# Optimization experiments

Measured on AMD Instinct MI355X. Metric: run time of the kernel, lower is better.

The kernel has to match this reference:

```python
import jax, jax.numpy as jnp
import numpy as np

GROUP_SIZE = 8
REQUIRED_ZEROS = 4


def _dorefa_quantize(x, bits):
    # tanh-normalize-round
    t = jnp.tanh(x).astype(jnp.float32)
    y = t / jnp.max(jnp.abs(t))
    delta = float(2 ** (bits - 1) - 1)
    _y = jnp.round(y * delta)

    out_c, in_c, h, w = _y.shape
    if in_c < GROUP_SIZE:
        return _y / delta

    g = in_c // GROUP_SIZE
    keep = GROUP_SIZE - REQUIRED_ZEROS  # keep at most 4 non-zeros per group

    # [out_c, g*8, h, w] -> [out_c, g, h, w, 8] (group axis last for top_k)
    yg = _y[:, : g * GROUP_SIZE].reshape(out_c, g, GROUP_SIZE, h, w)
    yg = jnp.transpose(yg, (0, 1, 3, 4, 2))

    # The torch loop zeroes the smallest-|v| non-zeros until >=4 zeros per
    # group. Equivalently: keep only the `keep` largest-|v| entries of each
    # group (zeros have |v|=0, so groups already having >=4 zeros are
    # unchanged). Fully vectorized via batched top-k + one-hot mask.
    absv = jnp.abs(yg)
    _, idx = jax.lax.top_k(absv, keep)                      # [o,g,h,w,keep]
    mask = jax.nn.one_hot(idx, GROUP_SIZE, dtype=yg.dtype).sum(axis=-2)
    yg = yg * mask                                          # [o,g,h,w,8]

    yg = jnp.transpose(yg, (0, 1, 4, 2, 3)).reshape(out_c, g * GROUP_SIZE, h, w)
    out = jnp.concatenate([yg, _y[:, g * GROUP_SIZE :]], axis=1) if g * GROUP_SIZE < in_c else yg
    return out / delta


def setup_inputs() -> dict:
    key = jax.random.key(0)
    x = jax.random.normal(key, (2048, 2048, 3, 3), dtype=jnp.float32)
    return {"x": x, "bits": 8}


def reference(x, bits):
    return _dorefa_quantize(x, bits)
```

## Files before the change

### kernel.cpp

```cpp
#include <hip/hip_runtime.h>
#include <math.h>

#define HW        9
#define GROUP     8
#define KEEP      4
#define DELTA     127.0f
#define INV_DELTA (1.0f / 127.0f)
#define GB_FLOATS 72

__global__ void maxabs_kernel(const float4* __restrict__ x, unsigned* __restrict__ ws, int n4) {
    __shared__ float red[4];
    float m = 0.0f;
    int stride = gridDim.x * blockDim.x;
    #pragma unroll 4
    for (int i = blockIdx.x * blockDim.x + threadIdx.x; i < n4; i += stride) {
        float4 v = x[i];
        m = fmaxf(m, fmaxf(fmaxf(fabsf(v.x), fabsf(v.y)),
                           fmaxf(fabsf(v.z), fabsf(v.w))));
    }
    #pragma unroll
    for (int off = 32; off > 0; off >>= 1)
        m = fmaxf(m, __shfl_down(m, off, 64));
    int wave = threadIdx.x >> 6;
    if ((threadIdx.x & 63) == 0) red[wave] = m;
    __syncthreads();
    if (threadIdx.x == 0) {
        float b = fmaxf(fmaxf(red[0], red[1]), fmaxf(red[2], red[3]));
        atomicMax(ws, __float_as_uint(b));
    }
}

__device__ __attribute__((noinline)) float ref_rz(float xx, float M) {
    float td = (float)tanh((double)xx);
    float y  = td / M;
    return rintf(y * DELTA);
}

__device__ __forceinline__ float fast_tanh(float x) {
    float ax  = fabsf(x);
    float axc = fminf(ax, 10.0f);
    float E   = __expf(2.0f * axc);
    float num = E - 1.0f;
    float den = E + 1.0f;
    float r0  = __builtin_amdgcn_rcpf(den);
    float r   = r0 * fmaf(-den, r0, 2.0f);
    float tl  = copysignf(num * r, x);
    float s = x * x;
    float p = fmaf(s, 0.0035921280f, -0.0088632358f);
    p = fmaf(s, p, 0.021869488f);
    p = fmaf(s, p, -0.053968254f);
    p = fmaf(s, p, 0.13333334f);
    p = fmaf(s, p, -0.33333334f);
    float ts = fmaf(x * s, p, x);
    return (ax <= 0.5f) ? ts : tl;
}

__global__ void quant_kernel(const float4* __restrict__ x,
                             float4* __restrict__ out,
                             const unsigned* __restrict__ ws,
                             int n_gb) {
    __shared__ float sM, sC;
    if (threadIdx.x == 0) {
        float mm = (float)tanh((double)__uint_as_float(*ws));
        sM = mm;
        sC = (float)(127.0 / (double)mm);
    }
    __syncthreads();
    float M = sM, C = sC;

    int gb = blockIdx.x * blockDim.x + threadIdx.x;
    if (gb >= n_gb) return;

    const float4* p = x   + (size_t)gb * (GB_FLOATS / 4);
    float4*       q = out + (size_t)gb * (GB_FLOATS / 4);

    float f[GB_FLOATS];
    #pragma unroll
    for (int k = 0; k < GB_FLOATS / 4; ++k) {
        float4 v = p[k];
        f[4 * k + 0] = v.x; f[4 * k + 1] = v.y;
        f[4 * k + 2] = v.z; f[4 * k + 3] = v.w;
    }

    #pragma unroll
    for (int hw = 0; hw < HW; ++hw) {
        float v8[GROUP], a8[GROUP];
        #pragma unroll
        for (int j = 0; j < GROUP; ++j) {
            float xx = f[j * HW + hw];
            float t  = fast_tanh(xx);
            float z  = t * C;
            float rz = rintf(z);
            float d  = 0.5f - fabsf(z - rz);
            if (d < fmaf(2e-6f, fabsf(z), 5e-7f))
                rz = ref_rz(xx, M);
            v8[j] = rz;
            a8[j] = fabsf(rz);
        }
        int rank[GROUP] = {0, 0, 0, 0, 0, 0, 0, 0};
        #pragma unroll
        for (int i = 0; i < GROUP; ++i) {
            #pragma unroll
            for (int j = i + 1; j < GROUP; ++j) {
                bool ge = (a8[i] >= a8[j]);
                rank[j] += ge ? 1 : 0;
                rank[i] += ge ? 0 : 1;
            }
        }
        #pragma unroll
        for (int j = 0; j < GROUP; ++j) {
            f[j * HW + hw] = (rank[j] < KEEP) ? (v8[j] * INV_DELTA) : 0.0f;
        }
    }

    #pragma unroll
    for (int k = 0; k < GB_FLOATS / 4; ++k) {
        float4 v;
        v.x = f[4 * k + 0]; v.y = f[4 * k + 1];
        v.z = f[4 * k + 2]; v.w = f[4 * k + 3];
        q[k] = v;
    }
}

extern "C" void kernel_launch(void* const* d_in, const int* in_sizes, int n_in,
                              void* d_out, int out_size, void* d_ws, size_t ws_size,
                              hipStream_t stream) {
    const float* x = (const float*)d_in[0];
    float* out = (float*)d_out;
    unsigned* ws = (unsigned*)d_ws;

    int n = in_sizes[0];
    int n4 = n / 4;
    int n_gb = n / GB_FLOATS;

    hipMemsetAsync(ws, 0, sizeof(unsigned), stream);

    maxabs_kernel<<<2048, 256, 0, stream>>>((const float4*)x, ws, n4);

    int blocks = (n_gb + 255) / 256;
    quant_kernel<<<blocks, 256, 0, stream>>>((const float4*)x, (float4*)out, ws, n_gb);
}
```

Before: 308.3 us.

## Stage quant kernel loads and stores through padded LDS for coalesced access

```diff
diff --git a/kernel.cpp b/kernel.cpp
--- a/kernel.cpp
+++ b/kernel.cpp
@@ -6,7 +6,9 @@
 #define KEEP      4
 #define DELTA     127.0f
 #define INV_DELTA (1.0f / 127.0f)
-#define GB_FLOATS 72
+#define ROW_F4    18
+#define ROW_PAD   19
+#define ROWS      256
 
 __global__ void maxabs_kernel(const float4* __restrict__ x, unsigned* __restrict__ ws, int n4) {
     __shared__ float red[4];
@@ -57,29 +59,35 @@
 
 __global__ void quant_kernel(const float4* __restrict__ x,
                              float4* __restrict__ out,
-                             const unsigned* __restrict__ ws,
-                             int n_gb) {
+                             const unsigned* __restrict__ ws) {
+    __shared__ float4 tile[ROWS * ROW_PAD];
     __shared__ float sM, sC;
     if (threadIdx.x == 0) {
         float mm = (float)tanh((double)__uint_as_float(*ws));
         sM = mm;
         sC = (float)(127.0 / (double)mm);
     }
+
+    int t = threadIdx.x;
+    size_t blk_f4 = (size_t)blockIdx.x * (ROWS * ROW_F4);
+
+    #pragma unroll
+    for (int k = 0; k < ROW_F4; ++k) {
+        int L = k * ROWS + t;
+        float4 v = x[blk_f4 + L];
+        int r = L / ROW_F4;
+        int e = L - r * ROW_F4;
+        tile[r * ROW_PAD + e] = v;
+    }
     __syncthreads();
     float M = sM, C = sC;
 
-    int gb = blockIdx.x * blockDim.x + threadIdx.x;
-    if (gb >= n_gb) return;
-
-    const float4* p = x   + (size_t)gb * (GB_FLOATS / 4);
-    float4*       q = out + (size_t)gb * (GB_FLOATS / 4);
-
-    float f[GB_FLOATS];
+    float f[ROWS ? 72 : 0];
     #pragma unroll
-    for (int k = 0; k < GB_FLOATS / 4; ++k) {
-        float4 v = p[k];
-        f[4 * k + 0] = v.x; f[4 * k + 1] = v.y;
-        f[4 * k + 2] = v.z; f[4 * k + 3] = v.w;
+    for (int e = 0; e < ROW_F4; ++e) {
+        float4 v = tile[t * ROW_PAD + e];
+        f[4 * e + 0] = v.x; f[4 * e + 1] = v.y;
+        f[4 * e + 2] = v.z; f[4 * e + 3] = v.w;
     }
 
     #pragma unroll
@@ -88,8 +96,8 @@
         #pragma unroll
         for (int j = 0; j < GROUP; ++j) {
             float xx = f[j * HW + hw];
-            float t  = fast_tanh(xx);
-            float z  = t * C;
+            float t1 = fast_tanh(xx);
+            float z  = t1 * C;
             float rz = rintf(z);
             float d  = 0.5f - fabsf(z - rz);
             if (d < fmaf(2e-6f, fabsf(z), 5e-7f))
@@ -114,11 +122,20 @@
     }
 
     #pragma unroll
-    for (int k = 0; k < GB_FLOATS / 4; ++k) {
+    for (int e = 0; e < ROW_F4; ++e) {
         float4 v;
-        v.x = f[4 * k + 0]; v.y = f[4 * k + 1];
-        v.z = f[4 * k + 2]; v.w = f[4 * k + 3];
-        q[k] = v;
+        v.x = f[4 * e + 0]; v.y = f[4 * e + 1];
+        v.z = f[4 * e + 2]; v.w = f[4 * e + 3];
+        tile[t * ROW_PAD + e] = v;
+    }
+    __syncthreads();
+
+    #pragma unroll
+    for (int k = 0; k < ROW_F4; ++k) {
+        int L = k * ROWS + t;
+        int r = L / ROW_F4;
+        int e = L - r * ROW_F4;
+        out[blk_f4 + L] = tile[r * ROW_PAD + e];
     }
 }
 
@@ -131,12 +148,12 @@
 
     int n = in_sizes[0];
     int n4 = n / 4;
-    int n_gb = n / GB_FLOATS;
+    int n_gb = n / 72;
 
     hipMemsetAsync(ws, 0, sizeof(unsigned), stream);
 
     maxabs_kernel<<<2048, 256, 0, stream>>>((const float4*)x, ws, n4);
 
-    int blocks = (n_gb + 255) / 256;
-    quant_kernel<<<blocks, 256, 0, stream>>>((const float4*)x, (float4*)out, ws, n_gb);
+    int blocks = n_gb / ROWS;
+    quant_kernel<<<blocks, 256, 0, stream>>>((const float4*)x, (float4*)out, ws);
 }
```

Result: slower. 317.0 us (+2.8%).
